# Performance work log

Hardware: AMD Instinct MI355X
Metric: run time of the kernel (lower is better)

## Reference

```python
import jax, jax.numpy as jnp
import numpy as np

DIM = 1024
CTX_DIM = 1024
HEADS = 8
DIM_HEAD = 64
INNER = HEADS * DIM_HEAD  # 512
EPS = 1e-5


def _layer_norm(x, gamma, beta):
    mu = jnp.mean(x, axis=-1, keepdims=True)
    var = jnp.mean(jnp.square(x - mu), axis=-1, keepdims=True)
    return (x - mu) * jax.lax.rsqrt(var + EPS) * gamma + beta


def setup_inputs() -> dict:
    key = jax.random.key(0)
    ks = jax.random.split(key, 8)
    b, n, m = 4, 2048, 2048
    x = jax.random.normal(ks[0], (b, n, DIM), dtype=jnp.float32)
    context = jax.random.normal(ks[1], (b, m, CTX_DIM), dtype=jnp.float32)
    Wq = jax.random.normal(ks[2], (DIM, INNER), dtype=jnp.float32) / np.sqrt(DIM)
    Wkv = jax.random.normal(ks[3], (CTX_DIM, 2 * INNER), dtype=jnp.float32) / np.sqrt(CTX_DIM)
    Wout = jax.random.normal(ks[4], (INNER, DIM), dtype=jnp.float32) / np.sqrt(INNER)
    bout = jnp.zeros((DIM,), dtype=jnp.float32)
    g1 = jnp.ones((DIM,), dtype=jnp.float32)
    b1 = jnp.zeros((DIM,), dtype=jnp.float32)
    g2 = jnp.ones((CTX_DIM,), dtype=jnp.float32)
    b2 = jnp.zeros((CTX_DIM,), dtype=jnp.float32)
    return {"x": x, "context": context, "g1": g1, "b1": b1, "g2": g2, "b2": b2,
            "Wq": Wq, "Wkv": Wkv, "Wout": Wout, "bout": bout}


def reference(x, context, g1, b1, g2, b2, Wq, Wkv, Wout, bout):
    b, n, _ = x.shape
    m = context.shape[1]
    scale = DIM_HEAD ** -0.5
    xn = _layer_norm(x, g1, b1)
    cn = _layer_norm(context, g2, b2)
    q = xn @ Wq                      # [b, n, inner]
    kv = cn @ Wkv                    # [b, m, 2*inner]
    k, v = jnp.split(kv, 2, axis=-1)
    # split heads: [b, h, seq, d]
    q = q.reshape(b, n, HEADS, DIM_HEAD).transpose(0, 2, 1, 3)
    k = k.reshape(b, m, HEADS, DIM_HEAD).transpose(0, 2, 1, 3)
    v = v.reshape(b, m, HEADS, DIM_HEAD).transpose(0, 2, 1, 3)
    sim = jnp.einsum('bhid,bhjd->bhij', q, k) * scale
    attn = jax.nn.softmax(sim, axis=-1)
    out = jnp.einsum('bhij,bhjd->bhid', attn, v)
    out = out.transpose(0, 2, 1, 3).reshape(b, n, INNER)
    return out @ Wout + bout
```

## Files before the change

kernel.cpp:

```cpp
#include <hip/hip_runtime.h>
#include <hip/hip_bf16.h>

typedef __bf16 bf16_t;
typedef bf16_t bf16x4 __attribute__((ext_vector_type(4)));
typedef bf16_t bf16x8 __attribute__((ext_vector_type(8)));
typedef float floatx4 __attribute__((ext_vector_type(4)));

typedef __attribute__((address_space(1))) const unsigned char* gptr_t;
typedef __attribute__((address_space(3))) unsigned char* lptr_t;

#define BATCH 4
#define SEQ_N 2048
#define SEQ_M 2048
#define DIM 1024
#define INNER 512
#define HEADS 8
#define DHEAD 64
#define QSCALE 0.18033688011112042f

#if __has_builtin(__builtin_amdgcn_exp2f)
#define fast_exp2(x) __builtin_amdgcn_exp2f(x)
#else
#define fast_exp2(x) exp2f(x)
#endif

__device__ __forceinline__ void wtrans_tile(const float* W, bf16_t* Wt,
                                            int K, int N, int n0, int k0, float scale) {
    __shared__ bf16_t T[64][72];
    const int tid = threadIdx.x;
#pragma unroll
    for (int p = 0; p < 2; p++) {
        int r = (tid >> 3) + p * 32;
        int c = (tid & 7) * 8;
        const float* src = W + (size_t)(k0 + r) * N + n0 + c;
        float4 v0 = *(const float4*)src;
        float4 v1 = *(const float4*)(src + 4);
        T[r][c + 0] = (bf16_t)(v0.x * scale); T[r][c + 1] = (bf16_t)(v0.y * scale);
        T[r][c + 2] = (bf16_t)(v0.z * scale); T[r][c + 3] = (bf16_t)(v0.w * scale);
        T[r][c + 4] = (bf16_t)(v1.x * scale); T[r][c + 5] = (bf16_t)(v1.y * scale);
        T[r][c + 6] = (bf16_t)(v1.z * scale); T[r][c + 7] = (bf16_t)(v1.w * scale);
    }
    __syncthreads();
#pragma unroll
    for (int p = 0; p < 2; p++) {
        int rn = (tid >> 3) + p * 32;
        int ck = (tid & 7) * 8;
        bf16x8 v;
#pragma unroll
        for (int i = 0; i < 8; i++) v[i] = T[ck + i][rn];
        *(bf16x8*)(Wt + (size_t)(n0 + rn) * K + k0 + ck) = v;
    }
}

__device__ __forceinline__ void ln_row_wave(const float* in, const float* g,
                                            const float* bt, bf16_t* out, int row) {
    const int lane = threadIdx.x & 63;
    const float4* src = (const float4*)(in + (size_t)row * 1024);
    float4 xv[4];
    float s = 0.f, ss = 0.f;
#pragma unroll
    for (int k = 0; k < 4; k++) {
        xv[k] = src[lane + k * 64];
        s  += xv[k].x + xv[k].y + xv[k].z + xv[k].w;
        ss += xv[k].x * xv[k].x + xv[k].y * xv[k].y + xv[k].z * xv[k].z + xv[k].w * xv[k].w;
    }
#pragma unroll
    for (int off = 32; off > 0; off >>= 1) {
        s  += __shfl_down(s, off);
        ss += __shfl_down(ss, off);
    }
    s  = __shfl(s, 0);
    ss = __shfl(ss, 0);
    const float mu = s * (1.f / 1024.f);
    const float var = ss * (1.f / 1024.f) - mu * mu;
    const float rs = rsqrtf(var + 1e-5f);
    const float4* gp = (const float4*)g;
    const float4* bp = (const float4*)bt;
#pragma unroll
    for (int k = 0; k < 4; k++) {
        float4 gv = gp[lane + k * 64], bv = bp[lane + k * 64];
        bf16x4 o;
        o[0] = (bf16_t)((xv[k].x - mu) * rs * gv.x + bv.x);
        o[1] = (bf16_t)((xv[k].y - mu) * rs * gv.y + bv.y);
        o[2] = (bf16_t)((xv[k].z - mu) * rs * gv.z + bv.z);
        o[3] = (bf16_t)((xv[k].w - mu) * rs * gv.w + bv.w);
        *(bf16x4*)(out + (size_t)row * 1024 + (lane + k * 64) * 4) = o;
    }
}

__global__ __launch_bounds__(256) void prep_kernel(const float* __restrict__ x,
                                                   const float* __restrict__ ctx,
                                                   const float* __restrict__ g1,
                                                   const float* __restrict__ b1,
                                                   const float* __restrict__ g2,
                                                   const float* __restrict__ b2,
                                                   const float* __restrict__ Wq,
                                                   const float* __restrict__ Wkv,
                                                   const float* __restrict__ Wout,
                                                   bf16_t* __restrict__ xn,
                                                   bf16_t* __restrict__ cn,
                                                   bf16_t* __restrict__ Wqt,
                                                   bf16_t* __restrict__ Wkvt,
                                                   bf16_t* __restrict__ Woutt) {
    int id = blockIdx.x;
    if (id < 128) {
        wtrans_tile(Wq, Wqt, 1024, 512, (id & 7) * 64, (id >> 3) * 64, QSCALE);
    } else if (id < 384) {
        int t = id - 128;
        wtrans_tile(Wkv, Wkvt, 1024, 1024, (t & 15) * 64, (t >> 4) * 64, 1.0f);
    } else if (id < 512) {
        int t = id - 384;
        wtrans_tile(Wout, Woutt, 512, 1024, (t & 15) * 64, (t >> 4) * 64, 1.0f);
    } else {
        int row = (id - 512) * 4 + (threadIdx.x >> 6);
        if (row < BATCH * SEQ_N) ln_row_wave(x, g1, b1, xn, row);
        else                     ln_row_wave(ctx, g2, b2, cn, row - BATCH * SEQ_N);
    }
}

template <int NT, int MODE, typename OutT>
__device__ __forceinline__ void gemm_body(const bf16_t* __restrict__ A,
                                          const bf16_t* __restrict__ Bt,
                                          OutT* __restrict__ C,
                                          const float* __restrict__ bias,
                                          int ldC, int K, int row0, int col0) {
    __shared__ bf16_t As[128 * 64];
    __shared__ bf16_t Bs[NT * 64];
    const int tid = threadIdx.x;
    const int wave = tid >> 6, lane = tid & 63;
    constexpr int WC = NT / 2;
    constexpr int NJ = WC / 16;
    const int wr = (wave >> 1) * 64, wc = (wave & 1) * WC;
    const int quad = lane >> 4, l16 = lane & 15;

    floatx4 acc[4][NJ] = {};

    for (int k0 = 0; k0 < K; k0 += 64) {
#pragma unroll
        for (int p = 0; p < 4; p++) {
            int cA = p * 256 + wave * 64 + lane;
            int rA = cA >> 3, kc = (cA & 7) * 8;
            __builtin_amdgcn_global_load_lds(
                (gptr_t)(A + (size_t)(row0 + rA) * K + k0 + kc),
                (lptr_t)(As + (size_t)(p * 256 + wave * 64) * 8), 16, 0, 0);
            if (p < NT / 32)
                __builtin_amdgcn_global_load_lds(
                    (gptr_t)(Bt + (size_t)(col0 + rA) * K + k0 + kc),
                    (lptr_t)(Bs + (size_t)(p * 256 + wave * 64) * 8), 16, 0, 0);
        }
        __syncthreads();
#pragma unroll
        for (int kt = 0; kt < 2; kt++) {
            bf16x8 aF[4], bF[NJ];
#pragma unroll
            for (int i = 0; i < 4; i++)
                aF[i] = *(bf16x8*)&As[(wr + i * 16 + l16) * 64 + kt * 32 + quad * 8];
#pragma unroll
            for (int j = 0; j < NJ; j++)
                bF[j] = *(bf16x8*)&Bs[(wc + j * 16 + l16) * 64 + kt * 32 + quad * 8];
#pragma unroll
            for (int i = 0; i < 4; i++)
#pragma unroll
                for (int j = 0; j < NJ; j++) {
                    if (MODE == 0)
                        acc[i][j] = __builtin_amdgcn_mfma_f32_16x16x32_bf16(
                            aF[i], bF[j], acc[i][j], 0, 0, 0);
                    else
                        acc[i][j] = __builtin_amdgcn_mfma_f32_16x16x32_bf16(
                            bF[j], aF[i], acc[i][j], 0, 0, 0);
                }
        }
        __syncthreads();
    }

    if (MODE == 0) {
#pragma unroll
        for (int i = 0; i < 4; i++)
#pragma unroll
            for (int j = 0; j < NJ; j++) {
                int col = col0 + wc + j * 16 + l16;
                float bv = bias ? bias[col] : 0.f;
#pragma unroll
                for (int r = 0; r < 4; r++) {
                    int row = row0 + wr + i * 16 + quad * 4 + r;
                    C[(size_t)row * ldC + col] = (OutT)(acc[i][j][r] + bv);
                }
            }
    } else {
        bf16_t* Tw = (wave < 2 ? As : Bs) + (wave & 1) * 4096;
#pragma unroll
        for (int i = 0; i < 4; i++)
#pragma unroll
            for (int j = 0; j < 4; j++)
#pragma unroll
                for (int r = 0; r < 4; r++)
                    Tw[(j * 16 + quad * 4 + r) * 64 + i * 16 + l16] = (bf16_t)acc[i][j][r];
        __syncthreads();
        const int grow = row0 + wr;
        const int bat = grow >> 11, gm = (grow & 2047) + l16 * 4;
#pragma unroll
        for (int dd = 0; dd < 16; dd++) {
            int d = dd * 4 + quad;
            bf16x4 v = *(bf16x4*)&Tw[d * 64 + l16 * 4];
            int gd = col0 + wc + d - 512;
            *(bf16x4*)(C + ((size_t)bat * 512 + gd) * 2048 + gm) = v;
        }
    }
}

__global__ __launch_bounds__(256) void gemm_qkv_kernel(const bf16_t* __restrict__ xn,
                                                       const bf16_t* __restrict__ cn,
                                                       const bf16_t* __restrict__ Wqt,
                                                       const bf16_t* __restrict__ Wkvt,
                                                       bf16_t* __restrict__ qb,
                                                       bf16_t* __restrict__ kvb,
                                                       bf16_t* __restrict__ Vtg) {
    const int f = blockIdx.x;
    const int lb = (f & 7) * 96 + (f >> 3);
    const int bx = lb % 12;
    const int row0 = (lb / 12) * 128;
    if (bx < 4)
        gemm_body<128, 0, bf16_t>(xn, Wqt, qb, nullptr, 512, DIM, row0, bx * 128);
    else if (bx < 8)
        gemm_body<128, 0, bf16_t>(cn, Wkvt, kvb, nullptr, 512, DIM, row0, (bx - 4) * 128);
    else
        gemm_body<128, 1, bf16_t>(cn, Wkvt, Vtg, nullptr, 0, DIM, row0, (bx - 4) * 128);
}

__global__ __launch_bounds__(256) void gemm_out_kernel(const bf16_t* __restrict__ ao,
                                                       const bf16_t* __restrict__ Woutt,
                                                       float* __restrict__ out,
                                                       const float* __restrict__ bias) {
    const int f = blockIdx.x;
    const int lb = (f & 7) * 128 + (f >> 3);
    gemm_body<64, 0, float>(ao, Woutt, out, bias, DIM, INNER,
                            (lb >> 4) * 128, (lb & 15) * 64);
}

__global__ __launch_bounds__(128) void attn_kernel(const bf16_t* __restrict__ q,
                                                   const bf16_t* __restrict__ kv,
                                                   const bf16_t* __restrict__ Vtg,
                                                   bf16_t* __restrict__ o) {
    __shared__ bf16_t Qs[64 * 64];
    __shared__ bf16_t Ks[2][64 * 64];
    __shared__ bf16_t Vs[2][64 * 64];

    const int f = blockIdx.x;
    const int lb = ((f & 7) << 7) | (f >> 3);
    const int b = lb >> 8, h = (lb >> 5) & 7;
    const int n0 = (lb & 31) * 64;

    const int tid = threadIdx.x;
    const int wave = tid >> 6, lane = tid & 63;
    const int quad = lane >> 4, l16 = lane & 15;
    const int swz = (l16 & 7) << 3;

    const int sr = tid >> 3;
    const int sc = (tid & 7) * 8;
    const int scs = sc ^ ((sr & 7) << 3);

#pragma unroll
    for (int p = 0; p < 4; p++) {
        int r = sr + p * 16;
        *(bf16x8*)&Qs[r * 64 + scs] =
            *(const bf16x8*)(q + (size_t)(b * SEQ_N + n0 + r) * INNER + h * DHEAD + sc);
    }

    bf16x8 bOnes;
    {
        bf16_t ov = (l16 == 0) ? (bf16_t)1.0f : (bf16_t)0.0f;
#pragma unroll
        for (int i = 0; i < 8; i++) bOnes[i] = ov;
    }

    const bf16_t* kp = kv + (size_t)(b * SEQ_M) * 512 + h * DHEAD + sc;
    const bf16_t* vp = Vtg + (size_t)((b * HEADS + h) * DHEAD) * SEQ_M + sc;
    bf16x8 kreg[4], vreg[4];
#pragma unroll
    for (int p = 0; p < 4; p++) {
        kreg[p] = *(const bf16x8*)(kp + (size_t)(sr + p * 16) * 512);
        vreg[p] = *(const bf16x8*)(vp + (size_t)(sr + p * 16) * SEQ_M);
    }
    __syncthreads();

    bf16x8 aQ0[2], aQ1[2];
#pragma unroll
    for (int kt = 0; kt < 2; kt++) {
        aQ0[kt] = *(bf16x8*)&Qs[(wave * 32 + l16) * 64 + ((kt * 32 + quad * 8) ^ swz)];
        aQ1[kt] = *(bf16x8*)&Qs[(wave * 32 + 16 + l16) * 64 + ((kt * 32 + quad * 8) ^ swz)];
    }

#pragma unroll
    for (int p = 0; p < 4; p++) {
        int r = sr + p * 16;
        *(bf16x8*)&Ks[0][r * 64 + scs] = kreg[p];
        *(bf16x8*)&Vs[0][r * 64 + scs] = vreg[p];
    }
    kp += 64 * 512;
    vp += 64;
#pragma unroll
    for (int p = 0; p < 4; p++) {
        kreg[p] = *(const bf16x8*)(kp + (size_t)(sr + p * 16) * 512);
        vreg[p] = *(const bf16x8*)(vp + (size_t)(sr + p * 16) * SEQ_M);
    }
    __syncthreads();

    bf16_t* Pw0 = Qs + wave * 2048;
    bf16_t* Pw1 = Pw0 + 1024;

    floatx4 oacc0[5] = {}, oacc1[5] = {};

    int cur = 0;
    for (int it = 0; it < SEQ_M / 64; ++it) {
#pragma unroll
        for (int p = 0; p < 4; p++) {
            int r = sr + p * 16;
            *(bf16x8*)&Ks[cur ^ 1][r * 64 + scs] = kreg[p];
            *(bf16x8*)&Vs[cur ^ 1][r * 64 + scs] = vreg[p];
        }
        kp += 64 * 512;
        vp += 64;
#pragma unroll
        for (int p = 0; p < 4; p++) {
            kreg[p] = *(const bf16x8*)(kp + (size_t)(sr + p * 16) * 512);
            vreg[p] = *(const bf16x8*)(vp + (size_t)(sr + p * 16) * SEQ_M);
        }

        floatx4 s0[4] = {}, s1[4] = {};
        __builtin_amdgcn_s_setprio(1);
#pragma unroll
        for (int kt = 0; kt < 2; kt++)
#pragma unroll
            for (int jt = 0; jt < 4; jt++) {
                bf16x8 aK = *(bf16x8*)&Ks[cur][(jt * 16 + l16) * 64 +
                                              ((kt * 32 + quad * 8) ^ swz)];
                s0[jt] = __builtin_amdgcn_mfma_f32_16x16x32_bf16(aK, aQ0[kt], s0[jt], 0, 0, 0);
                s1[jt] = __builtin_amdgcn_mfma_f32_16x16x32_bf16(aK, aQ1[kt], s1[jt], 0, 0, 0);
            }
        __builtin_amdgcn_s_setprio(0);

#pragma unroll
        for (int jt = 0; jt < 4; jt++) {
            bf16x4 pk0, pk1;
#pragma unroll
            for (int r = 0; r < 4; r++) {
                pk0[r] = (bf16_t)fast_exp2(s0[jt][r]);
                pk1[r] = (bf16_t)fast_exp2(s1[jt][r]);
            }
            int pc = (jt * 16 + quad * 4) ^ swz;
            *(bf16x4*)&Pw0[l16 * 64 + pc] = pk0;
            *(bf16x4*)&Pw1[l16 * 64 + pc] = pk1;
        }

        __builtin_amdgcn_s_setprio(1);
#pragma unroll
        for (int kt = 0; kt < 2; kt++) {
            int ac = (kt * 32 + quad * 8) ^ swz;
            bf16x8 aP0 = *(bf16x8*)&Pw0[l16 * 64 + ac];
            bf16x8 aP1 = *(bf16x8*)&Pw1[l16 * 64 + ac];
#pragma unroll
            for (int dt = 0; dt < 4; dt++) {
                bf16x8 bV = *(bf16x8*)&Vs[cur][(dt * 16 + l16) * 64 + ac];
                oacc0[dt] = __builtin_amdgcn_mfma_f32_16x16x32_bf16(aP0, bV, oacc0[dt], 0, 0, 0);
                oacc1[dt] = __builtin_amdgcn_mfma_f32_16x16x32_bf16(aP1, bV, oacc1[dt], 0, 0, 0);
            }
            oacc0[4] = __builtin_amdgcn_mfma_f32_16x16x32_bf16(aP0, bOnes, oacc0[4], 0, 0, 0);
            oacc1[4] = __builtin_amdgcn_mfma_f32_16x16x32_bf16(aP1, bOnes, oacc1[4], 0, 0, 0);
        }
        __builtin_amdgcn_s_setprio(0);
        __syncthreads();
        cur ^= 1;
    }

#pragma unroll
    for (int set = 0; set < 2; set++) {
        const floatx4* oa = set == 0 ? oacc0 : oacc1;
        float inv[4];
#pragma unroll
        for (int r = 0; r < 4; r++) {
            float l = __shfl(oa[4][r], (int)(lane & 48));
            inv[r] = 1.0f / l;
        }
#pragma unroll
        for (int dt = 0; dt < 4; dt++)
#pragma unroll
            for (int r = 0; r < 4; r++) {
                int row = n0 + wave * 32 + set * 16 + quad * 4 + r;
                int col = h * DHEAD + dt * 16 + l16;
                o[(size_t)(b * SEQ_N + row) * INNER + col] =
                    (bf16_t)(oa[dt][r] * inv[r]);
            }
    }
}

extern "C" void kernel_launch(void* const* d_in, const int* in_sizes, int n_in,
                              void* d_out, int out_size, void* d_ws, size_t ws_size,
                              hipStream_t stream) {
    const float* x    = (const float*)d_in[0];
    const float* ctx  = (const float*)d_in[1];
    const float* g1   = (const float*)d_in[2];
    const float* b1   = (const float*)d_in[3];
    const float* g2   = (const float*)d_in[4];
    const float* b2   = (const float*)d_in[5];
    const float* Wq   = (const float*)d_in[6];
    const float* Wkv  = (const float*)d_in[7];
    const float* Wout = (const float*)d_in[8];
    const float* bout = (const float*)d_in[9];
    float* out = (float*)d_out;

    const int rows = BATCH * SEQ_N;
    bf16_t* xn    = (bf16_t*)d_ws;
    bf16_t* cn    = xn + (size_t)rows * DIM;
    bf16_t* qb    = cn + (size_t)rows * DIM;
    bf16_t* kvb   = qb + (size_t)rows * INNER;
    bf16_t* Vtg   = kvb + (size_t)rows * INNER;
    bf16_t* Wqt   = Vtg + (size_t)rows * INNER;
    bf16_t* Wkvt  = Wqt + (size_t)INNER * DIM;
    bf16_t* Woutt = Wkvt + (size_t)(2 * INNER) * DIM;
    bf16_t* o_attn = xn;

    prep_kernel<<<512 + (2 * rows) / 4, 256, 0, stream>>>(
        x, ctx, g1, b1, g2, b2, Wq, Wkv, Wout, xn, cn, Wqt, Wkvt, Woutt);
    gemm_qkv_kernel<<<768, 256, 0, stream>>>(
        xn, cn, Wqt, Wkvt, qb, kvb, Vtg);
    attn_kernel<<<1024, 128, 0, stream>>>(qb, kvb, Vtg, o_attn);
    gemm_out_kernel<<<1024, 256, 0, stream>>>(o_attn, Woutt, out, bout);
}
```

Before: 243.9 us.

## Stream K/V tiles directly into LDS with global_load_lds

Replaces the register-staged K/V prefetch (global load into VGPRs, then an LDS store) with __builtin_amdgcn_global_load_lds transfers that write straight into the double-buffered LDS tiles. The XOR swizzle moves from the LDS store address to the global source column. The next tile is now issued right after the end-of-iteration barrier into the buffer just freed. The aim is to save VGPRs and LDS store instructions and to overlap the K/V fetch with MFMA work. The risks are visibility and ordering: there is no explicit vmcnt wait before the LDS reads, and the last prefetches read past the end of the sequence.

```diff
diff --git a/kernel.cpp b/kernel.cpp
--- a/kernel.cpp
+++ b/kernel.cpp
@@ -259,6 +259,23 @@
     const int sc = (tid & 7) * 8;
     const int scs = sc ^ ((sr & 7) << 3);
 
+    const int rloc = lane >> 3;
+    const int srccol = ((lane & 7) ^ rloc) << 3;
+    const bf16_t* kgl = kv + ((size_t)(b * SEQ_M) + wave * 32 + rloc) * 512
+                           + h * DHEAD + srccol;
+    const bf16_t* vgl = Vtg + ((size_t)((b * HEADS + h) * DHEAD)
+                               + wave * 32 + rloc) * SEQ_M + srccol;
+
+#pragma unroll
+    for (int p = 0; p < 4; p++) {
+        __builtin_amdgcn_global_load_lds(
+            (gptr_t)(kgl + (size_t)(p * 8) * 512),
+            (lptr_t)(Ks[0] + (wave * 4 + p) * 512), 16, 0, 0);
+        __builtin_amdgcn_global_load_lds(
+            (gptr_t)(vgl + (size_t)(p * 8) * SEQ_M),
+            (lptr_t)(Vs[0] + (wave * 4 + p) * 512), 16, 0, 0);
+    }
+
 #pragma unroll
     for (int p = 0; p < 4; p++) {
         int r = sr + p * 16;
@@ -273,14 +290,6 @@
         for (int i = 0; i < 8; i++) bOnes[i] = ov;
     }
 
-    const bf16_t* kp = kv + (size_t)(b * SEQ_M) * 512 + h * DHEAD + sc;
-    const bf16_t* vp = Vtg + (size_t)((b * HEADS + h) * DHEAD) * SEQ_M + sc;
-    bf16x8 kreg[4], vreg[4];
-#pragma unroll
-    for (int p = 0; p < 4; p++) {
-        kreg[p] = *(const bf16x8*)(kp + (size_t)(sr + p * 16) * 512);
-        vreg[p] = *(const bf16x8*)(vp + (size_t)(sr + p * 16) * SEQ_M);
-    }
     __syncthreads();
 
     bf16x8 aQ0[2], aQ1[2];
@@ -290,20 +299,17 @@
         aQ1[kt] = *(bf16x8*)&Qs[(wave * 32 + 16 + l16) * 64 + ((kt * 32 + quad * 8) ^ swz)];
     }
 
+    kgl += (size_t)64 * 512;
+    vgl += 64;
 #pragma unroll
     for (int p = 0; p < 4; p++) {
-        int r = sr + p * 16;
-        *(bf16x8*)&Ks[0][r * 64 + scs] = kreg[p];
-        *(bf16x8*)&Vs[0][r * 64 + scs] = vreg[p];
-    }
-    kp += 64 * 512;
-    vp += 64;
-#pragma unroll
-    for (int p = 0; p < 4; p++) {
-        kreg[p] = *(const bf16x8*)(kp + (size_t)(sr + p * 16) * 512);
-        vreg[p] = *(const bf16x8*)(vp + (size_t)(sr + p * 16) * SEQ_M);
-    }
-    __syncthreads();
+        __builtin_amdgcn_global_load_lds(
+            (gptr_t)(kgl + (size_t)(p * 8) * 512),
+            (lptr_t)(Ks[1] + (wave * 4 + p) * 512), 16, 0, 0);
+        __builtin_amdgcn_global_load_lds(
+            (gptr_t)(vgl + (size_t)(p * 8) * SEQ_M),
+            (lptr_t)(Vs[1] + (wave * 4 + p) * 512), 16, 0, 0);
+    }
 
     bf16_t* Pw0 = Qs + wave * 2048;
     bf16_t* Pw1 = Pw0 + 1024;
@@ -312,20 +318,6 @@
 
     int cur = 0;
     for (int it = 0; it < SEQ_M / 64; ++it) {
-#pragma unroll
-        for (int p = 0; p < 4; p++) {
-            int r = sr + p * 16;
-            *(bf16x8*)&Ks[cur ^ 1][r * 64 + scs] = kreg[p];
-            *(bf16x8*)&Vs[cur ^ 1][r * 64 + scs] = vreg[p];
-        }
-        kp += 64 * 512;
-        vp += 64;
-#pragma unroll
-        for (int p = 0; p < 4; p++) {
-            kreg[p] = *(const bf16x8*)(kp + (size_t)(sr + p * 16) * 512);
-            vreg[p] = *(const bf16x8*)(vp + (size_t)(sr + p * 16) * SEQ_M);
-        }
-
         floatx4 s0[4] = {}, s1[4] = {};
         __builtin_amdgcn_s_setprio(1);
 #pragma unroll
@@ -368,7 +360,20 @@
             oacc1[4] = __builtin_amdgcn_mfma_f32_16x16x32_bf16(aP1, bOnes, oacc1[4], 0, 0, 0);
         }
         __builtin_amdgcn_s_setprio(0);
+
         __syncthreads();
+
+        kgl += (size_t)64 * 512;
+        vgl += 64;
+#pragma unroll
+        for (int p = 0; p < 4; p++) {
+            __builtin_amdgcn_global_load_lds(
+                (gptr_t)(kgl + (size_t)(p * 8) * 512),
+                (lptr_t)(Ks[cur] + (wave * 4 + p) * 512), 16, 0, 0);
+            __builtin_amdgcn_global_load_lds(
+                (gptr_t)(vgl + (size_t)(p * 8) * SEQ_M),
+                (lptr_t)(Vs[cur] + (wave * 4 + p) * 512), 16, 0, 0);
+        }
         cur ^= 1;
     }
 
```

After: 245.0 us. No clear change (+0.5%).
